# Performance work log

Hardware: AMD Instinct MI355X
Metric: run time of the kernel (lower is better)

The kernel has to match this reference:

```python
import jax, jax.numpy as jnp
import numpy as np

B, T, F, D, H, HD = 1, 16, 256, 768, 12, 64
NUM_LOOKBACK = 6  # remaining H - NUM_LOOKBACK heads are lookahead


def setup_inputs() -> dict:
    key = jax.random.key(0)
    ks = jax.random.split(key, 9)
    s = 0.02
    return {
        "x": jax.random.normal(ks[0], (B, T, F, D), dtype=jnp.float32),
        "Wq": jax.random.normal(ks[1], (H, D, HD), dtype=jnp.float32) * s,
        "bq": jax.random.normal(ks[2], (H, HD), dtype=jnp.float32) * s,
        "Wk": jax.random.normal(ks[3], (H, D, HD), dtype=jnp.float32) * s,
        "bk": jax.random.normal(ks[4], (H, HD), dtype=jnp.float32) * s,
        "Wv": jax.random.normal(ks[5], (H, D, HD), dtype=jnp.float32) * s,
        "bv": jax.random.normal(ks[6], (H, HD), dtype=jnp.float32) * s,
        "Wo": jax.random.normal(ks[7], (D, D), dtype=jnp.float32) * s,
        "bo": jax.random.normal(ks[8], (D,), dtype=jnp.float32) * s,
    }


def reference(x, Wq, bq, Wk, bk, Wv, bv, Wo, bo):
    b, t, f, d = x.shape
    tf = t * f
    xf = x.reshape(b, tf, d)

    # batched per-head projections: [b, h, n, hd]
    q = jnp.einsum('bnd,hdk->bhnk', xf, Wq) + bq[None, :, None, :]
    k = jnp.einsum('bnd,hdk->bhnk', xf, Wk) + bk[None, :, None, :]
    v = jnp.einsum('bnd,hdk->bhnk', xf, Wv) + bv[None, :, None, :]

    scale = 1.0 / jnp.sqrt(jnp.asarray(q.shape[-1], dtype=q.dtype))
    scores = jnp.einsum('bhqd,bhkd->bhqk', q, k) * scale  # [b,h,tf,tf]

    # lookback mask == causal (q_idx >= kv_idx); lookahead == anti-causal
    idx = jnp.arange(tf)
    causal = idx[:, None] >= idx[None, :]
    neg = jnp.finfo(scores.dtype).min
    s_lb = jnp.where(causal[None, None], scores[:, :NUM_LOOKBACK], neg)
    s_la = jnp.where(causal.T[None, None], scores[:, NUM_LOOKBACK:], neg)
    scores = jnp.concatenate([s_lb, s_la], axis=1)

    p = jax.nn.softmax(scores, axis=-1)
    o = jnp.einsum('bhqk,bhkd->bhqd', p, v)  # [b,h,tf,hd]
    o = o.transpose(0, 2, 1, 3).reshape(b, tf, d)  # concat heads on feature dim

    out = o @ Wo + bo
    return out.reshape(b, t, f, d)
```

## Files before the change

### kernel.cpp

```cpp
#include <hip/hip_runtime.h>
#include <hip/hip_bf16.h>

typedef __attribute__((ext_vector_type(4))) float f32x4;
typedef __attribute__((ext_vector_type(8))) short s16x8;
typedef __attribute__((ext_vector_type(4))) int i32x4;
typedef __attribute__((address_space(3))) unsigned char lds_t;
typedef __attribute__((address_space(1))) const unsigned char glob_t;

#define TFDIM 4096
#define DMODEL 768
#define NHEAD 12
#define HDIM 64
#define NLB 6

static __device__ __forceinline__ unsigned short f2bf(float f) {
    union { float f; unsigned u; } x; x.f = f;
    unsigned r = x.u + 0x7fff + ((x.u >> 16) & 1);
    return (unsigned short)(r >> 16);
}

static __device__ __forceinline__ float exp2_hw(float x) {
    float r;
    asm("v_exp_f32 %0, %1\n\ts_nop 0" : "=v"(r) : "v"(x));
    return r;
}

static __device__ __forceinline__ unsigned cvtpk_bf16(float lo, float hi) {
    unsigned r;
    asm("v_cvt_pk_bf16_f32 %0, %1, %2" : "=v"(r) : "v"(lo), "v"(hi));
    return r;
}

static __device__ __forceinline__ void xpose_pair(unsigned& a, unsigned& b) {
    asm volatile("v_permlane32_swap_b32 %0, %1" : "+v"(a), "+v"(b));
    asm volatile("v_permlane16_swap_b32 %0, %1" : "+v"(a), "+v"(b));
}

__global__ __launch_bounds__(256) void prep_kernel(
    const float* __restrict__ x, unsigned short* __restrict__ xb,
    const float* __restrict__ Wq, const float* __restrict__ Wk, const float* __restrict__ Wv,
    const float* __restrict__ bq, const float* __restrict__ bk, const float* __restrict__ bv,
    unsigned short* __restrict__ Wt, float* __restrict__ bias,
    const float* __restrict__ Wo, unsigned short* __restrict__ Wot,
    float* __restrict__ Lacc, float* __restrict__ Oacc) {
    __shared__ unsigned short tile[64][65];
    int b = blockIdx.x;
    int t = threadIdx.x;
    if (b < 432) {
        int qkv = b / 144, rem = b - qkv * 144, h = rem / 12, kt = rem - h * 12;
        const float* W = (qkv == 0) ? Wq : ((qkv == 1) ? Wk : Wv);
        int trow = t >> 2, tco = (t & 3) << 4;
        const float* src = &W[((size_t)h * 768 + kt * 64 + trow) * 64 + tco];
#pragma unroll
        for (int j = 0; j < 4; j++) {
            float4 v = *(const float4*)&src[j * 4];
            tile[trow][tco + j * 4 + 0] = f2bf(v.x);
            tile[trow][tco + j * 4 + 1] = f2bf(v.y);
            tile[trow][tco + j * 4 + 2] = f2bf(v.z);
            tile[trow][tco + j * 4 + 3] = f2bf(v.w);
        }
        if (kt == 0 && t < 64) {
            const float* bb = (qkv == 0) ? bq : ((qkv == 1) ? bk : bv);
            bias[qkv * 768 + h * 64 + t] = bb[h * 64 + t];
        }
        __syncthreads();
        unsigned short vals[16];
#pragma unroll
        for (int j = 0; j < 16; j++) vals[j] = tile[tco + j][trow];
        unsigned short* dst = &Wt[(size_t)(qkv * 768 + h * 64 + trow) * 768 + kt * 64 + tco];
        *(s16x8*)&dst[0] = *(const s16x8*)&vals[0];
        *(s16x8*)&dst[8] = *(const s16x8*)&vals[8];
    } else if (b < 576) {
        int bb = b - 432;
        int nt = bb / 12, kt = bb - nt * 12;
        int trow = t >> 2, tco = (t & 3) << 4;
        const float* src = &Wo[(size_t)(kt * 64 + trow) * 768 + nt * 64 + tco];
#pragma unroll
        for (int j = 0; j < 4; j++) {
            float4 v = *(const float4*)&src[j * 4];
            tile[trow][tco + j * 4 + 0] = f2bf(v.x);
            tile[trow][tco + j * 4 + 1] = f2bf(v.y);
            tile[trow][tco + j * 4 + 2] = f2bf(v.z);
            tile[trow][tco + j * 4 + 3] = f2bf(v.w);
        }
        __syncthreads();
        unsigned short vals[16];
#pragma unroll
        for (int j = 0; j < 16; j++) vals[j] = tile[tco + j][trow];
        unsigned short* dst = &Wot[(size_t)(nt * 64 + trow) * 768 + kt * 64 + tco];
        *(s16x8*)&dst[0] = *(const s16x8*)&vals[0];
        *(s16x8*)&dst[8] = *(const s16x8*)&vals[8];
    } else if (b < 624) {
        int i = (b - 576) * 256 + t;
        if (i < NHEAD * TFDIM / 4) {
            float4 z = {0.f, 0.f, 0.f, 0.f};
            ((float4*)Lacc)[i] = z;
        }
    } else if (b < 3696) {
        int i = (b - 624) * 256 + t;
        if (i < TFDIM * DMODEL / 4) {
            float4 v = ((const float4*)x)[i];
            ushort4 o;
            o.x = f2bf(v.x); o.y = f2bf(v.y); o.z = f2bf(v.z); o.w = f2bf(v.w);
            ((ushort4*)xb)[i] = o;
        }
    } else {
        int i = (b - 3696) * 256 + t;
        if (i < TFDIM * DMODEL / 4) {
            float4 z = {0.f, 0.f, 0.f, 0.f};
            ((float4*)Oacc)[i] = z;
        }
    }
}

template <int EPI, int ANORM>
__global__ __launch_bounds__(256) void gemm_bt_kernel(
    const unsigned short* __restrict__ A,
    const float* __restrict__ Af32, const float* __restrict__ Lacc,
    const unsigned short* __restrict__ Bt,
    const float* __restrict__ bias,
    float* __restrict__ Cf, unsigned short* __restrict__ Cb,
    unsigned short* __restrict__ Vtg,
    int M, int N, int K) {
    __shared__ __align__(16) unsigned short As[128 * 64];
    __shared__ __align__(16) unsigned short Bs[128 * 64];
    int tid = threadIdx.x;
    int w = tid >> 6, l = tid & 63, lr = l & 15, lg = l >> 4;
    int wm = w >> 1, wn = w & 1;

    int nwg = gridDim.x * gridDim.y;
    int flat = blockIdx.y * gridDim.x + blockIdx.x;
    int cpx = nwg >> 3;
    int swz = (flat & 7) * cpx + (flat >> 3);
    int bx = swz % gridDim.x, by = swz / gridDim.x;
    size_t mbase = (size_t)by * 128, nbase = (size_t)bx * 128;

    int drw = l >> 3, dslot = l & 7;
    int dg = (dslot ^ drw) << 3;
    f32x4 acc[4][4] = {};
    for (int k0 = 0; k0 < K; k0 += 64) {
        __syncthreads();
        if (ANORM) {
#pragma unroll
            for (int i = 0; i < 4; i++) {
                int idx = tid + i * 256;
                int row = idx >> 3, g = idx & 7;
                const float* src = &Af32[(mbase + row) * K + k0 + g * 8];
                float4 a0 = *(const float4*)&src[0];
                float4 a1 = *(const float4*)&src[4];
                float rl = __builtin_amdgcn_rcpf(Lacc[(size_t)(k0 >> 6) * TFDIM + mbase + row]);
                unsigned short us[8];
                us[0] = f2bf(a0.x * rl); us[1] = f2bf(a0.y * rl);
                us[2] = f2bf(a0.z * rl); us[3] = f2bf(a0.w * rl);
                us[4] = f2bf(a1.x * rl); us[5] = f2bf(a1.y * rl);
                us[6] = f2bf(a1.z * rl); us[7] = f2bf(a1.w * rl);
                *(s16x8*)&As[row * 64 + ((g ^ (row & 7)) << 3)] = *(const s16x8*)us;
            }
        } else {
#pragma unroll
            for (int j = 0; j < 4; j++) {
                int row = j * 32 + w * 8 + drw;
                __builtin_amdgcn_global_load_lds((glob_t*)&A[(mbase + row) * K + k0 + dg],
                                                 (lds_t*)&As[(j * 32 + w * 8) * 64], 16, 0, 0);
            }
        }
#pragma unroll
        for (int j = 0; j < 4; j++) {
            int row = j * 32 + w * 8 + drw;
            __builtin_amdgcn_global_load_lds((glob_t*)&Bt[(nbase + row) * K + k0 + dg],
                                             (lds_t*)&Bs[(j * 32 + w * 8) * 64], 16, 0, 0);
        }
        __syncthreads();
#pragma unroll
        for (int ks = 0; ks < 2; ks++) {
            s16x8 af[4], bfr[4];
#pragma unroll
            for (int m = 0; m < 4; m++) {
                int row = wm * 64 + m * 16 + lr;
                af[m] = *(const s16x8*)&As[row * 64 + (((ks * 4 + lg) ^ (row & 7)) << 3)];
            }
#pragma unroll
            for (int n = 0; n < 4; n++) {
                int row = wn * 64 + n * 16 + lr;
                bfr[n] = *(const s16x8*)&Bs[row * 64 + (((ks * 4 + lg) ^ (row & 7)) << 3)];
            }
#pragma unroll
            for (int m = 0; m < 4; m++)
#pragma unroll
                for (int n = 0; n < 4; n++)
                    acc[m][n] = __builtin_amdgcn_mfma_f32_16x16x32_bf16(af[m], bfr[n], acc[m][n], 0, 0, 0);
        }
    }
    if (EPI == 1 && nbase >= 1536) {
        __syncthreads();
        unsigned short* L = (w < 2) ? &As[w * 4096] : &Bs[(w - 2) * 4096];
#pragma unroll
        for (int n = 0; n < 4; n++) {
            int dloc = n * 16 + lr;
            float bv = bias[nbase + wn * 64 + dloc];
            int sw = (dloc & 7) << 3;
#pragma unroll
            for (int m = 0; m < 4; m++) {
                int tokloc = m * 16 + lg * 4;
                uint2 pw;
                pw.x = cvtpk_bf16(acc[m][n][0] + bv, acc[m][n][1] + bv);
                pw.y = cvtpk_bf16(acc[m][n][2] + bv, acc[m][n][3] + bv);
                *(uint2*)&L[dloc * 64 + (tokloc ^ sw)] = pw;
            }
        }
        __asm__ volatile("" ::: "memory");
        int hq = ((int)(nbase - 1536) >> 6) + wn;
        size_t vbase = (size_t)hq * 262144 + mbase + wm * 64;
#pragma unroll
        for (int it = 0; it < 8; it++) {
            int dl = it * 8 + (l >> 3);
            int t0 = (l & 7) * 8;
            s16x8 vv = *(const s16x8*)&L[dl * 64 + (t0 ^ ((dl & 7) << 3))];
            *(s16x8*)&Vtg[vbase + (size_t)dl * 4096 + t0] = vv;
        }
    } else {
#pragma unroll
        for (int m = 0; m < 4; m++) {
            size_t row0 = mbase + wm * 64 + m * 16 + lg * 4;
#pragma unroll
            for (int n = 0; n < 4; n++) {
                size_t col = nbase + wn * 64 + n * 16 + lr;
                float bv = bias[col];
#pragma unroll
                for (int r = 0; r < 4; r++) {
                    float v = acc[m][n][r] + bv;
                    if (EPI == 0) {
                        Cf[(row0 + r) * N + col] = v;
                    } else {
                        if (col < 768) v *= 0.18033688f;
                        Cb[(((col >> 6) * 4096 + (row0 + r)) << 6) + (col & 63)] = f2bf(v);
                    }
                }
            }
        }
    }
}

__global__ __launch_bounds__(512, 4) void attn_kernel(const unsigned short* __restrict__ qk,
                                                      const unsigned short* __restrict__ vtg,
                                                      float* __restrict__ Oacc,
                                                      float* __restrict__ Lacc) {
    __shared__ __align__(16) unsigned short Ks[3][64][64];
    __shared__ __align__(16) unsigned short Vs[3][64][64];

    int b = blockIdx.x;
    int h = b % NHEAD;
    int idx = 79 - (b / NHEAD);
    int jqw, c, n;
    if (idx < 8)       { jqw = idx;               c = 0;              n = 1; }
    else if (idx < 24) { jqw = 8 + ((idx - 8) >> 1);  c = (idx - 8) & 1;  n = 2; }
    else if (idx < 48) { jqw = 16 + (idx - 24) / 3;   c = (idx - 24) % 3; n = 3; }
    else               { jqw = 24 + ((idx - 48) >> 2); c = (idx - 48) & 3; n = 4; }
    int W = 2 * jqw + 2;
    int base = W / n, rem = W % n;
    int len = base + (c < rem ? 1 : 0);
    int s0 = c * base + (c < rem ? c : rem);
    bool causal = (h < NLB);
    int jq = causal ? jqw : (31 - jqw);
    int qbase = jq * 128;
    int dkb = 2 * jq;
    int kb0 = (causal ? 0 : (62 - 2 * jqw)) + s0;
    int kb1 = kb0 + len - 1;

    const unsigned short* Q  = qk + (size_t)h * TFDIM * HDIM;
    const unsigned short* Kp = qk + (size_t)(NHEAD + h) * TFDIM * HDIM;
    const unsigned short* Vt = vtg + (size_t)h * HDIM * TFDIM;

    int tid = threadIdx.x, w = tid >> 6, l = tid & 63, lr = l & 15, lg = l >> 4;
    int qh = w >> 2, wq = w & 3;
    int dk = dkb + qh;

    s16x8 qf[2];
    {
        size_t qrow = (size_t)(qbase + qh * 64 + wq * 16 + lr);
        qf[0] = *(const s16x8*)&Q[qrow * HDIM + lg * 8];
        qf[1] = *(const s16x8*)&Q[qrow * HDIM + 32 + lg * 8];
    }
    f32x4 oacc[4] = {};
    float lsum = 0.f;

    int drow = tid >> 3, dseg = tid & 7;
    int sg0 = (dseg ^ (drow & 7)) << 3;
    auto stage = [&](int buf, int kv) {
        __builtin_amdgcn_global_load_lds((glob_t*)(Kp + (size_t)(kv * 64 + drow) * HDIM + sg0),
                                         (lds_t*)&Ks[buf][w * 8][0], 16, 0, 0);
        __builtin_amdgcn_global_load_lds((glob_t*)(Vt + (size_t)drow * TFDIM + kv * 64 + sg0),
                                         (lds_t*)&Vs[buf][w * 8][0], 16, 0, 0);
    };

    stage(0, kb0);

    int cur = 0;
    int qcol = wq * 16 + lr;
    for (int kb = kb0; kb <= kb1; kb++) {
        bool more = (kb < kb1);
        if (more) {
            int nxt = (cur == 2) ? 0 : cur + 1;
            stage(nxt, kb + 1);
            asm volatile("s_waitcnt vmcnt(2)" ::: "memory");
        } else {
            asm volatile("s_waitcnt vmcnt(0)" ::: "memory");
        }
        __builtin_amdgcn_s_barrier();
        __builtin_amdgcn_sched_barrier(0);

        int kvbase = kb * 64;
        s16x8 vf[2][4];
#pragma unroll
        for (int ks = 0; ks < 2; ks++)
#pragma unroll
            for (int df = 0; df < 4; df++)
                vf[ks][df] = *(const s16x8*)&Vs[cur][df * 16 + lr][(ks * 32 + lg * 8) ^ ((lr & 7) << 3)];
        f32x4 s[4];
        __builtin_amdgcn_s_setprio(1);
#pragma unroll
        for (int f = 0; f < 4; f++) {
            s16x8 kf0 = *(const s16x8*)&Ks[cur][f * 16 + lr][(lg * 8) ^ ((lr & 7) << 3)];
            s16x8 kf1 = *(const s16x8*)&Ks[cur][f * 16 + lr][(32 + lg * 8) ^ ((lr & 7) << 3)];
            f32x4 z = {0.f, 0.f, 0.f, 0.f};
            z = __builtin_amdgcn_mfma_f32_16x16x32_bf16(kf0, qf[0], z, 0, 0, 0);
            z = __builtin_amdgcn_mfma_f32_16x16x32_bf16(kf1, qf[1], z, 0, 0, 0);
            s[f] = z;
        }
        __builtin_amdgcn_s_setprio(0);

        bool skip = causal ? (kb > dk) : (kb < dk);
        if (!skip) {
            if (kb == dk) {
                int qi = qbase + qh * 64 + qcol;
#pragma unroll
                for (int f = 0; f < 4; f++)
#pragma unroll
                    for (int r = 0; r < 4; r++) {
                        int ki = kvbase + f * 16 + lg * 4 + r;
                        bool keep = causal ? (qi >= ki) : (qi <= ki);
                        if (!keep) s[f][r] = -1e30f;
                    }
            }
            float ls = 0.f;
            unsigned w0[4], w1[4];
#pragma unroll
            for (int f = 0; f < 4; f++) {
                float p0 = exp2_hw(s[f][0]);
                float p1 = exp2_hw(s[f][1]);
                float p2 = exp2_hw(s[f][2]);
                float p3 = exp2_hw(s[f][3]);
                ls += (p0 + p1) + (p2 + p3);
                w0[f] = cvtpk_bf16(p0, p1);
                w1[f] = cvtpk_bf16(p2, p3);
            }
            lsum += ls;
            xpose_pair(w0[0], w0[1]);
            xpose_pair(w1[0], w1[1]);
            xpose_pair(w0[2], w0[3]);
            xpose_pair(w1[2], w1[3]);
            union { unsigned u[4]; s16x8 v8; } pk0, pk1;
            pk0.u[0] = w0[0]; pk0.u[1] = w1[0]; pk0.u[2] = w0[1]; pk0.u[3] = w1[1];
            pk1.u[0] = w0[2]; pk1.u[1] = w1[2]; pk1.u[2] = w0[3]; pk1.u[3] = w1[3];
            __builtin_amdgcn_s_setprio(1);
#pragma unroll
            for (int df = 0; df < 4; df++) {
                oacc[df] = __builtin_amdgcn_mfma_f32_16x16x32_bf16(pk0.v8, vf[0][df], oacc[df], 0, 0, 0);
                oacc[df] = __builtin_amdgcn_mfma_f32_16x16x32_bf16(pk1.v8, vf[1][df], oacc[df], 0, 0, 0);
            }
            __builtin_amdgcn_s_setprio(0);
        }

        cur = (cur == 2) ? 0 : cur + 1;
    }
    lsum += __shfl_xor(lsum, 16);
    lsum += __shfl_xor(lsum, 32);
    if (lg == 0)
        atomicAdd(&Lacc[h * TFDIM + qbase + qh * 64 + wq * 16 + lr], lsum);
#pragma unroll
    for (int df = 0; df < 4; df++)
#pragma unroll
        for (int r = 0; r < 4; r++) {
            int row = qbase + qh * 64 + wq * 16 + lg * 4 + r;
            atomicAdd(&Oacc[(size_t)row * DMODEL + h * HDIM + df * 16 + lr], oacc[df][r]);
        }
}

__global__ void merge_kernel(const float* __restrict__ Oacc, const float* __restrict__ Lacc,
                             unsigned short* __restrict__ ob) {
    int i = blockIdx.x * 256 + threadIdx.x;
    if (i >= TFDIM * DMODEL / 4) return;
    int col4 = i % (DMODEL / 4), row = i / (DMODEL / 4);
    float4 v = ((const float4*)Oacc)[i];
    int h = col4 >> 4;
    float rl = 1.0f / Lacc[h * TFDIM + row];
    ushort4 u;
    u.x = f2bf(v.x * rl); u.y = f2bf(v.y * rl); u.z = f2bf(v.z * rl); u.w = f2bf(v.w * rl);
    ((ushort4*)ob)[i] = u;
}


extern "C" void kernel_launch(void* const* d_in, const int* in_sizes, int n_in,
                              void* d_out, int out_size, void* d_ws, size_t ws_size,
                              hipStream_t stream) {
    const float* x  = (const float*)d_in[0];
    const float* Wq = (const float*)d_in[1];
    const float* bq = (const float*)d_in[2];
    const float* Wk = (const float*)d_in[3];
    const float* bk = (const float*)d_in[4];
    const float* Wv = (const float*)d_in[5];
    const float* bv = (const float*)d_in[6];
    const float* Wo = (const float*)d_in[7];
    const float* bo = (const float*)d_in[8];
    float* out = (float*)d_out;
    char* ws = (char*)d_ws;
    const unsigned short* dummyA = (const unsigned short*)d_ws;

    if (ws_size >= 45416448) {
        unsigned short* xb   = (unsigned short*)(ws + 0);
        unsigned short* WtQ  = (unsigned short*)(ws + 6291456);
        float*          bqkv = (float*)(ws + 9830400);
        unsigned short* qkb  = (unsigned short*)(ws + 12582912);
        unsigned short* ob2  = (unsigned short*)(ws + 12582912);
        unsigned short* vtg  = (unsigned short*)(ws + 25165824);
        unsigned short* Wot  = (unsigned short*)(ws + 31457280);
        float*          Lacc = (float*)(ws + 32636928);
        float*          Oacc = (float*)(ws + 32833536);

        prep_kernel<<<6768, 256, 0, stream>>>(x, xb, Wq, Wk, Wv, bq, bk, bv, WtQ, bqkv, Wo, Wot, Lacc, Oacc);

        dim3 g1(2304 / 128, 4096 / 128);
        gemm_bt_kernel<1, 0><<<g1, 256, 0, stream>>>(xb, nullptr, nullptr, WtQ, bqkv, nullptr, qkb, vtg, 4096, 2304, 768);

        attn_kernel<<<960, 512, 0, stream>>>(qkb, vtg, Oacc, Lacc);

        merge_kernel<<<(TFDIM * DMODEL / 4 + 255) / 256, 256, 0, stream>>>(Oacc, Lacc, ob2);

        dim3 g3(768 / 128, 4096 / 128);
        gemm_bt_kernel<0, 0><<<g3, 256, 0, stream>>>(ob2, nullptr, nullptr, Wot, bo, out, nullptr, nullptr, 4096, 768, 768);
    } else if (ws_size >= 32833536) {
        float*          Oacc = (float*)(ws + 0);
        unsigned short* xb   = (unsigned short*)(ws + 0);
        unsigned short* WtQ  = (unsigned short*)(ws + 6291456);
        float*          bqkv = (float*)(ws + 9830400);
        unsigned short* qkb  = (unsigned short*)(ws + 12582912);
        unsigned short* ob2  = (unsigned short*)(ws + 12582912);
        unsigned short* vtg  = (unsigned short*)(ws + 25165824);
        unsigned short* Wot  = (unsigned short*)(ws + 31457280);
        float*          Lacc = (float*)(ws + 32636928);

        prep_kernel<<<3696, 256, 0, stream>>>(x, xb, Wq, Wk, Wv, bq, bk, bv, WtQ, bqkv, Wo, Wot, Lacc, nullptr);

        dim3 g1(2304 / 128, 4096 / 128);
        gemm_bt_kernel<1, 0><<<g1, 256, 0, stream>>>(xb, nullptr, nullptr, WtQ, bqkv, nullptr, qkb, vtg, 4096, 2304, 768);

        hipMemsetAsync(Oacc, 0, (size_t)TFDIM * DMODEL * 4, stream);

        attn_kernel<<<960, 512, 0, stream>>>(qkb, vtg, Oacc, Lacc);

        merge_kernel<<<(TFDIM * DMODEL / 4 + 255) / 256, 256, 0, stream>>>(Oacc, Lacc, ob2);

        dim3 g3(768 / 128, 4096 / 128);
        gemm_bt_kernel<0, 0><<<g3, 256, 0, stream>>>(ob2, nullptr, nullptr, Wot, bo, out, nullptr, nullptr, 4096, 768, 768);
    } else {
        unsigned short* xb   = (unsigned short*)(ws + 0);
        unsigned short* ob   = (unsigned short*)(ws + 0);
        unsigned short* WtQ  = (unsigned short*)(ws + 6291456);
        unsigned short* Wot  = (unsigned short*)(ws + 9830400);
        float*          bqkv = (float*)(ws + 11010048);
        unsigned short* qkb  = (unsigned short*)(ws + 11019264);
        unsigned short* vtg  = (unsigned short*)(ws + 23602176);
        float*          Lacc = (float*)(ws + 29893632);
        float*          Oacc = out;

        hipMemsetAsync(Oacc, 0, (size_t)TFDIM * DMODEL * 4, stream);
        prep_kernel<<<3696, 256, 0, stream>>>(x, xb, Wq, Wk, Wv, bq, bk, bv, WtQ, bqkv, Wo, Wot, Lacc, nullptr);

        dim3 g1(2304 / 128, 4096 / 128);
        gemm_bt_kernel<1, 0><<<g1, 256, 0, stream>>>(xb, nullptr, nullptr, WtQ, bqkv, nullptr, qkb, vtg, 4096, 2304, 768);

        attn_kernel<<<960, 512, 0, stream>>>(qkb, vtg, Oacc, Lacc);
        merge_kernel<<<(TFDIM * DMODEL / 4 + 255) / 256, 256, 0, stream>>>(Oacc, Lacc, ob);

        dim3 g3(768 / 128, 4096 / 128);
        gemm_bt_kernel<0, 0><<<g3, 256, 0, stream>>>(ob, nullptr, nullptr, Wot, bo, out, nullptr, nullptr, 4096, 768, 768);
    }
}
```

Measured before the change: 119.4 us.

## Replace fp32 atomic split-KV output accumulation with per-split bf16 partial buffers

Instead of atomically adding fp32 partial attention outputs into a zeroed accumulator, each split-KV chunk writes its unnormalized output as bf16 into its own slot buffer. A new merge kernel sums the up-to-four partials per row, divides by the row's softmax denominator and writes bf16. This removes the fp32 atomics and the prep kernel's zeroing of the Oacc region (the prep launch shrinks). The cost is extra bf16 rounding of the partial sums and a merge that reads several partial buffers.

```diff
diff --git a/kernel.cpp b/kernel.cpp
--- a/kernel.cpp
+++ b/kernel.cpp
@@ -12,11 +12,16 @@
 #define NHEAD 12
 #define HDIM 64
 #define NLB 6
+#define SLOTSZ 3145728
 
 static __device__ __forceinline__ unsigned short f2bf(float f) {
     union { float f; unsigned u; } x; x.f = f;
     unsigned r = x.u + 0x7fff + ((x.u >> 16) & 1);
     return (unsigned short)(r >> 16);
+}
+
+static __device__ __forceinline__ float bf2f(unsigned short u) {
+    return __uint_as_float(((unsigned)u) << 16);
 }
 
 static __device__ __forceinline__ float exp2_hw(float x) {
@@ -241,10 +246,13 @@
     }
 }
 
+template <int PART>
 __global__ __launch_bounds__(512, 4) void attn_kernel(const unsigned short* __restrict__ qk,
                                                       const unsigned short* __restrict__ vtg,
                                                       float* __restrict__ Oacc,
-                                                      float* __restrict__ Lacc) {
+                                                      float* __restrict__ Lacc,
+                                                      unsigned short* __restrict__ PO01,
+                                                      unsigned short* __restrict__ PO23) {
     __shared__ __align__(16) unsigned short Ks[3][64][64];
     __shared__ __align__(16) unsigned short Vs[3][64][64];
 
@@ -377,13 +385,25 @@
     lsum += __shfl_xor(lsum, 32);
     if (lg == 0)
         atomicAdd(&Lacc[h * TFDIM + qbase + qh * 64 + wq * 16 + lr], lsum);
-#pragma unroll
-    for (int df = 0; df < 4; df++)
-#pragma unroll
-        for (int r = 0; r < 4; r++) {
-            int row = qbase + qh * 64 + wq * 16 + lg * 4 + r;
-            atomicAdd(&Oacc[(size_t)row * DMODEL + h * HDIM + df * 16 + lr], oacc[df][r]);
-        }
+    if (PART) {
+        unsigned short* PO = (c < 2) ? (PO01 + (size_t)c * SLOTSZ)
+                                     : (PO23 + (size_t)(c - 2) * SLOTSZ);
+#pragma unroll
+        for (int df = 0; df < 4; df++)
+#pragma unroll
+            for (int r = 0; r < 4; r++) {
+                int row = qbase + qh * 64 + wq * 16 + lg * 4 + r;
+                PO[((size_t)h * TFDIM + row) * 64 + df * 16 + lr] = f2bf(oacc[df][r]);
+            }
+    } else {
+#pragma unroll
+        for (int df = 0; df < 4; df++)
+#pragma unroll
+            for (int r = 0; r < 4; r++) {
+                int row = qbase + qh * 64 + wq * 16 + lg * 4 + r;
+                atomicAdd(&Oacc[(size_t)row * DMODEL + h * HDIM + df * 16 + lr], oacc[df][r]);
+            }
+    }
 }
 
 __global__ void merge_kernel(const float* __restrict__ Oacc, const float* __restrict__ Lacc,
@@ -397,6 +417,33 @@
     ushort4 u;
     u.x = f2bf(v.x * rl); u.y = f2bf(v.y * rl); u.z = f2bf(v.z * rl); u.w = f2bf(v.w * rl);
     ((ushort4*)ob)[i] = u;
+}
+
+__global__ void merge_part_kernel(const unsigned short* __restrict__ PO01,
+                                  const unsigned short* __restrict__ PO23,
+                                  const float* __restrict__ Lacc,
+                                  unsigned short* __restrict__ ob) {
+    int i = blockIdx.x * 256 + threadIdx.x;
+    if (i >= TFDIM * 96) return;
+    int row = i / 96, g = i - row * 96;
+    int h = g >> 3, c0 = (g & 7) << 3;
+    int jq = row >> 7;
+    int jqw = (h < NLB) ? jq : (31 - jq);
+    int n = 1 + (jqw >> 3);
+    size_t off = ((size_t)h * TFDIM + row) * 64 + c0;
+    float acc[8] = {};
+    for (int s = 0; s < n; s++) {
+        const unsigned short* PO = (s < 2) ? (PO01 + (size_t)s * SLOTSZ)
+                                           : (PO23 + (size_t)(s - 2) * SLOTSZ);
+        s16x8 v = *(const s16x8*)&PO[off];
+#pragma unroll
+        for (int j = 0; j < 8; j++) acc[j] += bf2f((unsigned short)v[j]);
+    }
+    float rl = 1.0f / Lacc[h * TFDIM + row];
+    unsigned short o8[8];
+#pragma unroll
+    for (int j = 0; j < 8; j++) o8[j] = f2bf(acc[j] * rl);
+    *(s16x8*)&ob[(size_t)row * DMODEL + h * HDIM + c0] = *(const s16x8*)o8;
 }
 
 
@@ -417,24 +464,25 @@
     const unsigned short* dummyA = (const unsigned short*)d_ws;
 
     if (ws_size >= 45416448) {
-        unsigned short* xb   = (unsigned short*)(ws + 0);
-        unsigned short* WtQ  = (unsigned short*)(ws + 6291456);
-        float*          bqkv = (float*)(ws + 9830400);
-        unsigned short* qkb  = (unsigned short*)(ws + 12582912);
-        unsigned short* ob2  = (unsigned short*)(ws + 12582912);
-        unsigned short* vtg  = (unsigned short*)(ws + 25165824);
-        unsigned short* Wot  = (unsigned short*)(ws + 31457280);
-        float*          Lacc = (float*)(ws + 32636928);
-        float*          Oacc = (float*)(ws + 32833536);
-
-        prep_kernel<<<6768, 256, 0, stream>>>(x, xb, Wq, Wk, Wv, bq, bk, bv, WtQ, bqkv, Wo, Wot, Lacc, Oacc);
+        unsigned short* xb     = (unsigned short*)(ws + 0);
+        unsigned short* PO01   = (unsigned short*)(ws + 0);
+        unsigned short* WtQ    = (unsigned short*)(ws + 6291456);
+        float*          bqkv   = (float*)(ws + 9830400);
+        unsigned short* qkb    = (unsigned short*)(ws + 12582912);
+        unsigned short* ob2    = (unsigned short*)(ws + 12582912);
+        unsigned short* vtg    = (unsigned short*)(ws + 25165824);
+        unsigned short* Wot    = (unsigned short*)(ws + 31457280);
+        float*          Lacc   = (float*)(ws + 32636928);
+        unsigned short* PO23   = (unsigned short*)(ws + 32833536);
+
+        prep_kernel<<<3696, 256, 0, stream>>>(x, xb, Wq, Wk, Wv, bq, bk, bv, WtQ, bqkv, Wo, Wot, Lacc, nullptr);
 
         dim3 g1(2304 / 128, 4096 / 128);
         gemm_bt_kernel<1, 0><<<g1, 256, 0, stream>>>(xb, nullptr, nullptr, WtQ, bqkv, nullptr, qkb, vtg, 4096, 2304, 768);
 
-        attn_kernel<<<960, 512, 0, stream>>>(qkb, vtg, Oacc, Lacc);
-
-        merge_kernel<<<(TFDIM * DMODEL / 4 + 255) / 256, 256, 0, stream>>>(Oacc, Lacc, ob2);
+        attn_kernel<1><<<960, 512, 0, stream>>>(qkb, vtg, nullptr, Lacc, PO01, PO23);
+
+        merge_part_kernel<<<(TFDIM * 96 + 255) / 256, 256, 0, stream>>>(PO01, PO23, Lacc, ob2);
 
         dim3 g3(768 / 128, 4096 / 128);
         gemm_bt_kernel<0, 0><<<g3, 256, 0, stream>>>(ob2, nullptr, nullptr, Wot, bo, out, nullptr, nullptr, 4096, 768, 768);
@@ -456,7 +504,7 @@
 
         hipMemsetAsync(Oacc, 0, (size_t)TFDIM * DMODEL * 4, stream);
 
-        attn_kernel<<<960, 512, 0, stream>>>(qkb, vtg, Oacc, Lacc);
+        attn_kernel<0><<<960, 512, 0, stream>>>(qkb, vtg, Oacc, Lacc, nullptr, nullptr);
 
         merge_kernel<<<(TFDIM * DMODEL / 4 + 255) / 256, 256, 0, stream>>>(Oacc, Lacc, ob2);
 
@@ -479,7 +527,7 @@
         dim3 g1(2304 / 128, 4096 / 128);
         gemm_bt_kernel<1, 0><<<g1, 256, 0, stream>>>(xb, nullptr, nullptr, WtQ, bqkv, nullptr, qkb, vtg, 4096, 2304, 768);
 
-        attn_kernel<<<960, 512, 0, stream>>>(qkb, vtg, Oacc, Lacc);
+        attn_kernel<0><<<960, 512, 0, stream>>>(qkb, vtg, Oacc, Lacc, nullptr, nullptr);
         merge_kernel<<<(TFDIM * DMODEL / 4 + 255) / 256, 256, 0, stream>>>(Oacc, Lacc, ob);
 
         dim3 g3(768 / 128, 4096 / 128);
```

Result: faster. 108.2 us (-9.4%).
